# Optimization experiments

Measured on AMD Instinct MI355X. Metric: run time of the kernel, lower is better.

The kernel has to match this reference:

```python
import jax, jax.numpy as jnp
import numpy as np
from math import sqrt

H = 16  # num_heads
E = 1024  # embedding_size
B, S = 2, 2048

def setup_inputs() -> dict:
    key = jax.random.key(0)
    ks = jax.random.split(key, 12)
    sc = 1.0 / sqrt(E)
    inp = {
        'q': jax.random.normal(ks[0], (B, S, E), jnp.float32),
        'k': jax.random.normal(ks[1], (B, S, E), jnp.float32),
        'v': jax.random.normal(ks[2], (B, S, E), jnp.float32),
        'Wq': jax.random.normal(ks[3], (E, E), jnp.float32) * sc,
        'bq': jnp.zeros((E,), jnp.float32),
        'Wk': jax.random.normal(ks[4], (E, E), jnp.float32) * sc,
        'bk': jnp.zeros((E,), jnp.float32),
        'Wv': jax.random.normal(ks[5], (E, E), jnp.float32) * sc,
        'bv': jnp.zeros((E,), jnp.float32),
        'Wo': jax.random.normal(ks[6], (E, E), jnp.float32) * sc,
        'bo': jnp.zeros((E,), jnp.float32),
        'gamma': jnp.ones((E,), jnp.float32),
        'beta': jnp.zeros((E,), jnp.float32),
        'attn_mask': jnp.tril(jnp.ones((S, S), jnp.int32))[None, None],  # causal [1,1,S,S]
        'pad_mask': jnp.ones((B, S), jnp.int32),
    }
    return inp


def reference(q, k, v, Wq, bq, Wk, bk, Wv, bv, Wo, bo, gamma, beta, attn_mask, pad_mask):
    hs = E // H
    residual = q
    # NOTE: faithful to original: contiguous view(-1, H, S, hs) reinterprets
    # [B, S, E] memory directly as [B, H, S, hs] (no transpose).
    qh = (q @ Wq + bq).reshape(B, H, S, hs)
    kh = (k @ Wk + bk).reshape(B, H, S, hs)
    vh = (v @ Wv + bv).reshape(B, H, S, hs)
    scores = jnp.einsum('bhqd,bhkd->bhqk', qh, kh)  # [B,H,Sq,Sk]
    neg_inf = jnp.float32(-jnp.inf)
    scores = jnp.where(pad_mask[:, None, None, :] == 0, neg_inf, scores)
    scores = jnp.where(attn_mask == 0, neg_inf, scores)
    attn = jax.nn.softmax(scores / sqrt(hs), axis=-1)
    out = jnp.einsum('bhqk,bhkd->bhqd', attn, vh).reshape(B, S, E)
    out = out @ Wo + bo  # dropout is identity at inference
    x = residual + out
    mean = jnp.mean(x, axis=-1, keepdims=True)
    std = jnp.sqrt(jnp.mean((x - mean) ** 2, axis=-1, keepdims=True))  # unbiased=False
    return gamma * ((x - mean) / (std + 1e-8)) + beta
```

## Files before the change

### kernel.cpp

```cpp
#include <hip/hip_runtime.h>
#include <hip/hip_bf16.h>
#include <stdint.h>
#include <math.h>

#define NH 16
#define E_ 1024
#define B_ 2
#define S_ 2048
#define HS 64
#define M_TOT (B_*S_)

typedef __attribute__((ext_vector_type(4))) float f32x4;
typedef __attribute__((ext_vector_type(8))) short short8;

static __device__ __forceinline__ short f2bf(float f) {
    union { __hip_bfloat16 h; short s; } u;
    u.h = __float2bfloat16(f);
    return u.s;
}

static __device__ __forceinline__ void glds16(const void* g, void* l) {
    __builtin_amdgcn_global_load_lds(
        (__attribute__((address_space(1))) void*)(g),
        (__attribute__((address_space(3))) void*)(l),
        16, 0, 0);
}

__global__ __launch_bounds__(256) void cvt_qkv(
    const float* __restrict__ q, const float* __restrict__ k, const float* __restrict__ v,
    short* __restrict__ qb, short* __restrict__ kb, short* __restrict__ vb)
{
    const float* src; short* dst;
    if (blockIdx.y == 0)      { src = q; dst = qb; }
    else if (blockIdx.y == 1) { src = k; dst = kb; }
    else                      { src = v; dst = vb; }
    int i = (blockIdx.x * 256 + threadIdx.x) * 4;
    float4 f = *(const float4*)(src + i);
    short4 o;
    o.x = f2bf(f.x); o.y = f2bf(f.y); o.z = f2bf(f.z); o.w = f2bf(f.w);
    *(short4*)(dst + i) = o;
}

__global__ __launch_bounds__(256) void transpose_w4(
    const float* __restrict__ Wq, const float* __restrict__ Wk,
    const float* __restrict__ Wv, const float* __restrict__ Wo,
    short* __restrict__ Wqt, short* __restrict__ Wkt,
    short* __restrict__ Wvt, short* __restrict__ Wot)
{
    __shared__ float tile[32][33];
    const float* W; short* Wt;
    switch (blockIdx.z) {
        case 0: W = Wq; Wt = Wqt; break;
        case 1: W = Wk; Wt = Wkt; break;
        case 2: W = Wv; Wt = Wvt; break;
        default: W = Wo; Wt = Wot; break;
    }
    int tx = threadIdx.x, ty = threadIdx.y;
    int n0 = blockIdx.x * 32, k0 = blockIdx.y * 32;
#pragma unroll
    for (int i = 0; i < 4; i++)
        tile[ty + 8*i][tx] = W[(size_t)(k0 + ty + 8*i) * E_ + n0 + tx];
    __syncthreads();
#pragma unroll
    for (int i = 0; i < 4; i++)
        Wt[(size_t)(n0 + ty + 8*i) * E_ + k0 + tx] = f2bf(tile[tx][ty + 8*i]);
}

__global__ __launch_bounds__(256) void transpose_v(
    const short* __restrict__ Vb, short* __restrict__ Vt_g)
{
    __shared__ short tile[32][34];
    int tx = threadIdx.x, ty = threadIdx.y;
    int bh = blockIdx.z;
    int s0 = blockIdx.x * 32, d0 = blockIdx.y * 32;
    const short* src = Vb + (size_t)bh * S_ * HS;
    short* dst = Vt_g + (size_t)bh * HS * S_;
#pragma unroll
    for (int i = 0; i < 4; i++)
        tile[ty + 8*i][tx] = src[(size_t)(s0 + ty + 8*i) * HS + d0 + tx];
    __syncthreads();
#pragma unroll
    for (int i = 0; i < 4; i++)
        dst[(size_t)(d0 + ty + 8*i) * S_ + s0 + tx] = tile[tx][ty + 8*i];
}

#define BM 128
#define BN 128
#define BK 32

template<bool RESID>
__device__ __forceinline__ void gemm_core(
    const short* __restrict__ A, const short* __restrict__ Bt,
    const float* __restrict__ bias, const float* __restrict__ resid,
    short* __restrict__ outb, float* __restrict__ outf,
    int mblk, int nblk)
{
    __shared__ __align__(16) short As[BM * BK];
    __shared__ __align__(16) short Bs[BN * BK];

    const int tid  = threadIdx.x;
    const int lane = tid & 63;
    const int w    = tid >> 6;
    const int wm   = w >> 1, wn = w & 1;
    const int l15  = lane & 15, quad = lane >> 4;
    const int N = E_, K = E_;

    f32x4 acc[4][4];
#pragma unroll
    for (int i = 0; i < 4; i++)
#pragma unroll
        for (int j = 0; j < 4; j++)
            acc[i][j] = (f32x4){0.f, 0.f, 0.f, 0.f};

    const int arow = tid >> 2;
    const int acol = (tid & 3) * 8;
    const int m0 = mblk * BM, n0 = nblk * BN;
    short* AsW0 = As + w * 512;
    short* AsW1 = As + 2048 + w * 512;
    short* BsW0 = Bs + w * 512;
    short* BsW1 = Bs + 2048 + w * 512;

    for (int k0 = 0; k0 < K; k0 += BK) {
        __syncthreads();
        glds16(A  + (size_t)(m0 + arow)      * K + k0 + acol, AsW0);
        glds16(A  + (size_t)(m0 + arow + 64) * K + k0 + acol, AsW1);
        glds16(Bt + (size_t)(n0 + arow)      * K + k0 + acol, BsW0);
        glds16(Bt + (size_t)(n0 + arow + 64) * K + k0 + acol, BsW1);
        __syncthreads();

        short8 af[4], bf[4];
#pragma unroll
        for (int i = 0; i < 4; i++)
            af[i] = *(const short8*)(As + (wm*64 + i*16 + l15) * BK + quad*8);
#pragma unroll
        for (int j = 0; j < 4; j++)
            bf[j] = *(const short8*)(Bs + (wn*64 + j*16 + l15) * BK + quad*8);
#pragma unroll
        for (int i = 0; i < 4; i++)
#pragma unroll
            for (int j = 0; j < 4; j++)
                acc[i][j] = __builtin_amdgcn_mfma_f32_16x16x32_bf16(af[i], bf[j], acc[i][j], 0, 0, 0);
    }

#pragma unroll
    for (int i = 0; i < 4; i++)
#pragma unroll
        for (int j = 0; j < 4; j++) {
            int col = n0 + wn*64 + j*16 + l15;
            float bcol = bias[col];
#pragma unroll
            for (int r = 0; r < 4; r++) {
                int row = m0 + wm*64 + i*16 + quad*4 + r;
                float vv = acc[i][j][r] + bcol;
                if (RESID) {
                    outf[(size_t)row * N + col] = vv + resid[(size_t)row * N + col];
                } else {
                    outb[(size_t)row * N + col] = f2bf(vv);
                }
            }
        }
}

__global__ __launch_bounds__(256) void gemm_qkv(
    const short* qb, const short* kb, const short* vb,
    const short* Wqt, const short* Wkt, const short* Wvt,
    const float* bq, const float* bk, const float* bv,
    short* Qb, short* Kb, short* Vb)
{
    const short *A, *Bt; const float* bias; short* out;
    switch (blockIdx.z) {
        case 0:  A = qb; Bt = Wqt; bias = bq; out = Qb; break;
        case 1:  A = kb; Bt = Wkt; bias = bk; out = Kb; break;
        default: A = vb; Bt = Wvt; bias = bv; out = Vb; break;
    }
    gemm_core<false>(A, Bt, bias, nullptr, out, nullptr, blockIdx.y, blockIdx.x);
}

__global__ __launch_bounds__(256) void gemm_out(
    const short* Ab, const short* Wot, const float* bo,
    const float* resid, float* xout)
{
    gemm_core<true>(Ab, Wot, bo, resid, nullptr, xout, blockIdx.y, blockIdx.x);
}

#define SP 72

__global__ __launch_bounds__(256, 4) void flash_attn(
    const short* __restrict__ Q, const short* __restrict__ K,
    const short* __restrict__ Vt_g, short* __restrict__ O)
{
    const int bh  = blockIdx.y;
    const int qt  = (blockIdx.x + bh) & 31;
    const int tid = threadIdx.x;
    const int lane = tid & 63, w = tid >> 6;
    const int l15 = lane & 15, quad = lane >> 4;

    __shared__ __align__(16) short Ks[64 * SP];
    __shared__ __align__(16) short Vt[64 * SP];
    __shared__ __align__(16) short Ps[4][16 * SP];
    short* myPs = Ps[w];

    const short* Qbase = Q + ((size_t)bh * S_ + qt * 64 + w * 16) * HS;
    const short* Kb0   = K + (size_t)bh * S_ * HS;
    const short* Vg    = Vt_g + (size_t)bh * HS * S_;

    const int r0 = tid >> 3, c0 = (tid & 7) * 8;
    const int r1 = (tid + 256) >> 3, c1 = c0;

    short8 qf[2];
    qf[0] = *(const short8*)(Qbase + l15 * HS + quad * 8);
    qf[1] = *(const short8*)(Qbase + l15 * HS + 32 + quad * 8);

    uint4 rk0, rk1, rv0, rv1;
    {
        const short* Kt = Kb0;
        rk0 = *(const uint4*)(Kt + tid * 8);
        rk1 = *(const uint4*)(Kt + (tid + 256) * 8);
        rv0 = *(const uint4*)(Vg + (size_t)r0 * S_ + c0);
        rv1 = *(const uint4*)(Vg + (size_t)r1 * S_ + c1);
    }

    f32x4 o_acc[4];
#pragma unroll
    for (int j = 0; j < 4; j++) o_acc[j] = (f32x4){0.f, 0.f, 0.f, 0.f};
    float lsum[4] = {0.f, 0.f, 0.f, 0.f};

    for (int kt = 0; kt <= qt; kt++) {
        __syncthreads();
        *(uint4*)(Ks + r0 * SP + c0) = rk0;
        *(uint4*)(Ks + r1 * SP + c1) = rk1;
        *(uint4*)(Vt + r0 * SP + c0) = rv0;
        *(uint4*)(Vt + r1 * SP + c1) = rv1;
        __syncthreads();

        if (kt < qt) {
            const short* Kt = Kb0 + (size_t)(kt + 1) * 64 * HS;
            rk0 = *(const uint4*)(Kt + tid * 8);
            rk1 = *(const uint4*)(Kt + (tid + 256) * 8);
            rv0 = *(const uint4*)(Vg + (size_t)r0 * S_ + (kt + 1) * 64 + c0);
            rv1 = *(const uint4*)(Vg + (size_t)r1 * S_ + (kt + 1) * 64 + c1);
        }

        f32x4 sc[4];
#pragma unroll
        for (int j = 0; j < 4; j++) sc[j] = (f32x4){0.f, 0.f, 0.f, 0.f};
#pragma unroll
        for (int ks = 0; ks < 2; ks++)
#pragma unroll
            for (int j = 0; j < 4; j++) {
                short8 bk_ = *(const short8*)(Ks + (j*16 + l15) * SP + ks*32 + quad*8);
                sc[j] = __builtin_amdgcn_mfma_f32_16x16x32_bf16(qf[ks], bk_, sc[j], 0, 0, 0);
            }

        const bool diag = (kt == qt);
#pragma unroll
        for (int r = 0; r < 4; r++) {
            int qrow = w*16 + quad*4 + r;
            float rs = 0.f;
#pragma unroll
            for (int j = 0; j < 4; j++) {
                float s = sc[j][r] * 0.125f;
                if (diag) { int kc = j*16 + l15; if (kc > qrow) s = -INFINITY; }
                float p = __expf(s);
                rs += p;
                myPs[(quad*4 + r) * SP + j*16 + l15] = f2bf(p);
            }
            lsum[r] += rs;
        }

        short8 ap[2];
        ap[0] = *(const short8*)(myPs + l15 * SP + quad*8);
        ap[1] = *(const short8*)(myPs + l15 * SP + 32 + quad*8);
#pragma unroll
        for (int ks = 0; ks < 2; ks++)
#pragma unroll
            for (int j2 = 0; j2 < 4; j2++) {
                short8 bv_ = *(const short8*)(Vt + (j2*16 + l15) * SP + ks*32 + quad*8);
                o_acc[j2] = __builtin_amdgcn_mfma_f32_16x16x32_bf16(ap[ks], bv_, o_acc[j2], 0, 0, 0);
            }
    }

#pragma unroll
    for (int r = 0; r < 4; r++) {
#pragma unroll
        for (int off = 1; off < 16; off <<= 1)
            lsum[r] += __shfl_xor(lsum[r], off);
    }

    short* Ob = O + ((size_t)bh * S_ + qt * 64 + w * 16) * HS;
#pragma unroll
    for (int r = 0; r < 4; r++) {
        float inv = 1.f / lsum[r];
#pragma unroll
        for (int j2 = 0; j2 < 4; j2++)
            Ob[(quad*4 + r) * HS + j2*16 + l15] = f2bf(o_acc[j2][r] * inv);
    }
}

__global__ __launch_bounds__(256) void layernorm_k(
    const float* __restrict__ x, const float* __restrict__ gamma,
    const float* __restrict__ beta, float* __restrict__ out)
{
    int row = blockIdx.x;
    int tid = threadIdx.x;
    const float* xr = x + (size_t)row * E_;
    float4 v = *(const float4*)(xr + tid * 4);

    float s = v.x + v.y + v.z + v.w;
#pragma unroll
    for (int off = 1; off < 64; off <<= 1) s += __shfl_xor(s, off);
    __shared__ float red[4];
    if ((tid & 63) == 0) red[tid >> 6] = s;
    __syncthreads();
    float mean = (red[0] + red[1] + red[2] + red[3]) * (1.f / E_);

    float dx0 = v.x - mean, dx1 = v.y - mean, dx2 = v.z - mean, dx3 = v.w - mean;
    float sq = dx0*dx0 + dx1*dx1 + dx2*dx2 + dx3*dx3;
#pragma unroll
    for (int off = 1; off < 64; off <<= 1) sq += __shfl_xor(sq, off);
    __syncthreads();
    if ((tid & 63) == 0) red[tid >> 6] = sq;
    __syncthreads();
    float var = (red[0] + red[1] + red[2] + red[3]) * (1.f / E_);
    float inv = 1.f / (sqrtf(var) + 1e-8f);

    float4 g = *(const float4*)(gamma + tid * 4);
    float4 b = *(const float4*)(beta + tid * 4);
    float4 o;
    o.x = g.x * dx0 * inv + b.x;
    o.y = g.y * dx1 * inv + b.y;
    o.z = g.z * dx2 * inv + b.z;
    o.w = g.w * dx3 * inv + b.w;
    *(float4*)(out + (size_t)row * E_ + tid * 4) = o;
}

extern "C" void kernel_launch(void* const* d_in, const int* in_sizes, int n_in,
                              void* d_out, int out_size, void* d_ws, size_t ws_size,
                              hipStream_t stream)
{
    const float* q     = (const float*)d_in[0];
    const float* k     = (const float*)d_in[1];
    const float* v     = (const float*)d_in[2];
    const float* Wq    = (const float*)d_in[3];
    const float* bq    = (const float*)d_in[4];
    const float* Wk    = (const float*)d_in[5];
    const float* bk    = (const float*)d_in[6];
    const float* Wv    = (const float*)d_in[7];
    const float* bv    = (const float*)d_in[8];
    const float* Wo    = (const float*)d_in[9];
    const float* bo    = (const float*)d_in[10];
    const float* gamma = (const float*)d_in[11];
    const float* beta  = (const float*)d_in[12];

    const size_t ACT = (size_t)M_TOT * E_;
    char* ws = (char*)d_ws;
    size_t off = 0;
    auto alloc = [&](size_t bytes) { char* p = ws + off; off += bytes; return p; };

    short* qb   = (short*)alloc(ACT * 2);
    short* kb   = (short*)alloc(ACT * 2);
    short* vb   = (short*)alloc(ACT * 2);
    short* Wqt  = (short*)alloc((size_t)E_ * E_ * 2);
    short* Wkt  = (short*)alloc((size_t)E_ * E_ * 2);
    short* Wvt  = (short*)alloc((size_t)E_ * E_ * 2);
    short* Wot  = (short*)alloc((size_t)E_ * E_ * 2);
    short* Qb   = (short*)alloc(ACT * 2);
    short* Kb   = (short*)alloc(ACT * 2);
    short* Vb   = (short*)alloc(ACT * 2);
    short* Ob   = (short*)alloc(ACT * 2);
    float* xb   = (float*)alloc(ACT * 4);
    short* Vt_g = qb;

    cvt_qkv<<<dim3(ACT / 4 / 256, 3), 256, 0, stream>>>(q, k, v, qb, kb, vb);
    transpose_w4<<<dim3(32, 32, 4), dim3(32, 8), 0, stream>>>(Wq, Wk, Wv, Wo, Wqt, Wkt, Wvt, Wot);
    gemm_qkv<<<dim3(E_ / BN, M_TOT / BM, 3), 256, 0, stream>>>(qb, kb, vb, Wqt, Wkt, Wvt,
                                                               bq, bk, bv, Qb, Kb, Vb);
    transpose_v<<<dim3(S_ / 32, HS / 32, B_ * NH), dim3(32, 8), 0, stream>>>(Vb, Vt_g);
    flash_attn<<<dim3(S_ / 64, B_ * NH), 256, 0, stream>>>(Qb, Kb, Vt_g, Ob);
    gemm_out<<<dim3(E_ / BN, M_TOT / BM), 256, 0, stream>>>(Ob, Wot, bo, q, xb);
    layernorm_k<<<M_TOT, 256, 0, stream>>>(xb, gamma, beta, (float*)d_out);
}
```

Measured before the change: 265.3 us.

## Enlarge attention Q tile to 128 rows and split-K the output GEMM

Flash attention now handles 128 query rows per block, 32 per wave, so each K/V tile loaded into LDS feeds twice as many MFMAs. Query tiles are also reordered across heads to balance the causal workload, and fully masked tiles are skipped per wave. The output projection is split along K into two partial GEMMs that double the grid, with bias and residual addition moved into the layernorm kernel. The cost is more registers, with launch bounds lowered to two blocks per SM, plus an extra fp32 partial buffer read by layernorm.

```diff
diff --git a/kernel.cpp b/kernel.cpp
--- a/kernel.cpp
+++ b/kernel.cpp
@@ -88,12 +88,12 @@
 #define BN 128
 #define BK 32
 
-template<bool RESID>
+template<int MODE>
 __device__ __forceinline__ void gemm_core(
     const short* __restrict__ A, const short* __restrict__ Bt,
-    const float* __restrict__ bias, const float* __restrict__ resid,
+    const float* __restrict__ bias,
     short* __restrict__ outb, float* __restrict__ outf,
-    int mblk, int nblk)
+    int mblk, int nblk, int kbeg, int kend)
 {
     __shared__ __align__(16) short As[BM * BK];
     __shared__ __align__(16) short Bs[BN * BK];
@@ -120,7 +120,7 @@
     short* BsW0 = Bs + w * 512;
     short* BsW1 = Bs + 2048 + w * 512;
 
-    for (int k0 = 0; k0 < K; k0 += BK) {
+    for (int k0 = kbeg; k0 < kend; k0 += BK) {
         __syncthreads();
         glds16(A  + (size_t)(m0 + arow)      * K + k0 + acol, AsW0);
         glds16(A  + (size_t)(m0 + arow + 64) * K + k0 + acol, AsW1);
@@ -147,15 +147,14 @@
 #pragma unroll
         for (int j = 0; j < 4; j++) {
             int col = n0 + wn*64 + j*16 + l15;
-            float bcol = bias[col];
+            float bcol = (MODE == 0) ? bias[col] : 0.f;
 #pragma unroll
             for (int r = 0; r < 4; r++) {
                 int row = m0 + wm*64 + i*16 + quad*4 + r;
-                float vv = acc[i][j][r] + bcol;
-                if (RESID) {
-                    outf[(size_t)row * N + col] = vv + resid[(size_t)row * N + col];
+                if (MODE == 0) {
+                    outb[(size_t)row * N + col] = f2bf(acc[i][j][r] + bcol);
                 } else {
-                    outb[(size_t)row * N + col] = f2bf(vv);
+                    outf[(size_t)row * N + col] = acc[i][j][r];
                 }
             }
         }
@@ -173,138 +172,172 @@
         case 1:  A = kb; Bt = Wkt; bias = bk; out = Kb; break;
         default: A = vb; Bt = Wvt; bias = bv; out = Vb; break;
     }
-    gemm_core<false>(A, Bt, bias, nullptr, out, nullptr, blockIdx.y, blockIdx.x);
-}
-
-__global__ __launch_bounds__(256) void gemm_out(
-    const short* Ab, const short* Wot, const float* bo,
-    const float* resid, float* xout)
-{
-    gemm_core<true>(Ab, Wot, bo, resid, nullptr, xout, blockIdx.y, blockIdx.x);
+    gemm_core<0>(A, Bt, bias, out, nullptr, blockIdx.y, blockIdx.x, 0, E_);
+}
+
+__global__ __launch_bounds__(256) void gemm_out_sk(
+    const short* Ab, const short* Wot, float* xb0, float* xb1)
+{
+    float* out = (blockIdx.z == 0) ? xb0 : xb1;
+    int kbeg = blockIdx.z * (E_ / 2);
+    gemm_core<1>(Ab, Wot, nullptr, nullptr, out, blockIdx.y, blockIdx.x, kbeg, kbeg + E_/2);
 }
 
 #define SP 72
 
-__global__ __launch_bounds__(256, 4) void flash_attn(
+__global__ __launch_bounds__(256, 2) void flash_attn(
     const short* __restrict__ Q, const short* __restrict__ K,
     const short* __restrict__ Vt_g, short* __restrict__ O)
 {
-    const int bh  = blockIdx.y;
-    const int qt  = (blockIdx.x + bh) & 31;
-    const int tid = threadIdx.x;
+    const int bh   = blockIdx.y;
+    const int base = (blockIdx.x + bh) & 15;
+    const int qt   = (bh & 16) ? (15 - base) : base;
+    const int tid  = threadIdx.x;
     const int lane = tid & 63, w = tid >> 6;
-    const int l15 = lane & 15, quad = lane >> 4;
+    const int l15  = lane & 15, quad = lane >> 4;
 
     __shared__ __align__(16) short Ks[64 * SP];
     __shared__ __align__(16) short Vt[64 * SP];
-    __shared__ __align__(16) short Ps[4][16 * SP];
+    __shared__ __align__(16) short Ps[4][32 * SP];
     short* myPs = Ps[w];
 
-    const short* Qbase = Q + ((size_t)bh * S_ + qt * 64 + w * 16) * HS;
+    const int row0 = qt * 128 + w * 32;
+    const short* Qbase = Q + ((size_t)bh * S_ + row0) * HS;
     const short* Kb0   = K + (size_t)bh * S_ * HS;
     const short* Vg    = Vt_g + (size_t)bh * HS * S_;
 
     const int r0 = tid >> 3, c0 = (tid & 7) * 8;
-    const int r1 = (tid + 256) >> 3, c1 = c0;
-
-    short8 qf[2];
-    qf[0] = *(const short8*)(Qbase + l15 * HS + quad * 8);
-    qf[1] = *(const short8*)(Qbase + l15 * HS + 32 + quad * 8);
-
-    uint4 rk0, rk1, rv0, rv1;
-    {
-        const short* Kt = Kb0;
-        rk0 = *(const uint4*)(Kt + tid * 8);
-        rk1 = *(const uint4*)(Kt + (tid + 256) * 8);
-        rv0 = *(const uint4*)(Vg + (size_t)r0 * S_ + c0);
-        rv1 = *(const uint4*)(Vg + (size_t)r1 * S_ + c1);
-    }
-
-    f32x4 o_acc[4];
-#pragma unroll
-    for (int j = 0; j < 4; j++) o_acc[j] = (f32x4){0.f, 0.f, 0.f, 0.f};
-    float lsum[4] = {0.f, 0.f, 0.f, 0.f};
-
-    for (int kt = 0; kt <= qt; kt++) {
+    const int r1 = r0 + 32;
+
+    short8 qf[2][2];
+#pragma unroll
+    for (int i = 0; i < 2; i++) {
+        qf[i][0] = *(const short8*)(Qbase + (i*16 + l15) * HS + quad * 8);
+        qf[i][1] = *(const short8*)(Qbase + (i*16 + l15) * HS + 32 + quad * 8);
+    }
+
+    const int ktmax = 2 * qt + 1;
+
+    uint4 rk0 = *(const uint4*)(Kb0 + tid * 8);
+    uint4 rk1 = *(const uint4*)(Kb0 + (tid + 256) * 8);
+    uint4 rv0 = *(const uint4*)(Vg + (size_t)r0 * S_ + c0);
+    uint4 rv1 = *(const uint4*)(Vg + (size_t)r1 * S_ + c0);
+
+    f32x4 o_acc[2][4];
+#pragma unroll
+    for (int i = 0; i < 2; i++)
+#pragma unroll
+        for (int j = 0; j < 4; j++) o_acc[i][j] = (f32x4){0.f, 0.f, 0.f, 0.f};
+    float lsum[2][4] = {{0.f,0.f,0.f,0.f},{0.f,0.f,0.f,0.f}};
+
+    for (int kt = 0; kt <= ktmax; kt++) {
         __syncthreads();
         *(uint4*)(Ks + r0 * SP + c0) = rk0;
-        *(uint4*)(Ks + r1 * SP + c1) = rk1;
+        *(uint4*)(Ks + r1 * SP + c0) = rk1;
         *(uint4*)(Vt + r0 * SP + c0) = rv0;
-        *(uint4*)(Vt + r1 * SP + c1) = rv1;
+        *(uint4*)(Vt + r1 * SP + c0) = rv1;
         __syncthreads();
 
-        if (kt < qt) {
+        if (kt < ktmax) {
             const short* Kt = Kb0 + (size_t)(kt + 1) * 64 * HS;
             rk0 = *(const uint4*)(Kt + tid * 8);
             rk1 = *(const uint4*)(Kt + (tid + 256) * 8);
             rv0 = *(const uint4*)(Vg + (size_t)r0 * S_ + (kt + 1) * 64 + c0);
-            rv1 = *(const uint4*)(Vg + (size_t)r1 * S_ + (kt + 1) * 64 + c1);
+            rv1 = *(const uint4*)(Vg + (size_t)r1 * S_ + (kt + 1) * 64 + c0);
         }
 
-        f32x4 sc[4];
-#pragma unroll
-        for (int j = 0; j < 4; j++) sc[j] = (f32x4){0.f, 0.f, 0.f, 0.f};
+        if (kt * 64 > row0 + 31) continue;
+
+        f32x4 sc[2][4];
+#pragma unroll
+        for (int i = 0; i < 2; i++)
+#pragma unroll
+            for (int j = 0; j < 4; j++) sc[i][j] = (f32x4){0.f, 0.f, 0.f, 0.f};
 #pragma unroll
         for (int ks = 0; ks < 2; ks++)
 #pragma unroll
             for (int j = 0; j < 4; j++) {
-                short8 bk_ = *(const short8*)(Ks + (j*16 + l15) * SP + ks*32 + quad*8);
-                sc[j] = __builtin_amdgcn_mfma_f32_16x16x32_bf16(qf[ks], bk_, sc[j], 0, 0, 0);
+                short8 kf = *(const short8*)(Ks + (j*16 + l15) * SP + ks*32 + quad*8);
+#pragma unroll
+                for (int i = 0; i < 2; i++)
+                    sc[i][j] = __builtin_amdgcn_mfma_f32_16x16x32_bf16(qf[i][ks], kf, sc[i][j], 0, 0, 0);
             }
 
-        const bool diag = (kt == qt);
+        const bool needmask = (kt * 64 + 63) > row0;
+#pragma unroll
+        for (int i = 0; i < 2; i++)
+#pragma unroll
+            for (int r = 0; r < 4; r++) {
+                int qrow = row0 + i*16 + quad*4 + r;
+                float rs = 0.f;
+#pragma unroll
+                for (int j = 0; j < 4; j++) {
+                    float s = sc[i][j][r] * 0.125f;
+                    if (needmask) { int kc = kt*64 + j*16 + l15; if (kc > qrow) s = -INFINITY; }
+                    float p = __expf(s);
+                    rs += p;
+                    myPs[(i*16 + quad*4 + r) * SP + j*16 + l15] = f2bf(p);
+                }
+                lsum[i][r] += rs;
+            }
+
+        short8 ap[2][2];
+#pragma unroll
+        for (int i = 0; i < 2; i++) {
+            ap[i][0] = *(const short8*)(myPs + (i*16 + l15) * SP + quad*8);
+            ap[i][1] = *(const short8*)(myPs + (i*16 + l15) * SP + 32 + quad*8);
+        }
+#pragma unroll
+        for (int ks = 0; ks < 2; ks++)
+#pragma unroll
+            for (int j2 = 0; j2 < 4; j2++) {
+                short8 vf = *(const short8*)(Vt + (j2*16 + l15) * SP + ks*32 + quad*8);
+#pragma unroll
+                for (int i = 0; i < 2; i++)
+                    o_acc[i][j2] = __builtin_amdgcn_mfma_f32_16x16x32_bf16(ap[i][ks], vf, o_acc[i][j2], 0, 0, 0);
+            }
+    }
+
+#pragma unroll
+    for (int i = 0; i < 2; i++)
 #pragma unroll
         for (int r = 0; r < 4; r++) {
-            int qrow = w*16 + quad*4 + r;
-            float rs = 0.f;
-#pragma unroll
-            for (int j = 0; j < 4; j++) {
-                float s = sc[j][r] * 0.125f;
-                if (diag) { int kc = j*16 + l15; if (kc > qrow) s = -INFINITY; }
-                float p = __expf(s);
-                rs += p;
-                myPs[(quad*4 + r) * SP + j*16 + l15] = f2bf(p);
-            }
-            lsum[r] += rs;
+#pragma unroll
+            for (int off = 1; off < 16; off <<= 1)
+                lsum[i][r] += __shfl_xor(lsum[i][r], off);
         }
 
-        short8 ap[2];
-        ap[0] = *(const short8*)(myPs + l15 * SP + quad*8);
-        ap[1] = *(const short8*)(myPs + l15 * SP + 32 + quad*8);
-#pragma unroll
-        for (int ks = 0; ks < 2; ks++)
-#pragma unroll
-            for (int j2 = 0; j2 < 4; j2++) {
-                short8 bv_ = *(const short8*)(Vt + (j2*16 + l15) * SP + ks*32 + quad*8);
-                o_acc[j2] = __builtin_amdgcn_mfma_f32_16x16x32_bf16(ap[ks], bv_, o_acc[j2], 0, 0, 0);
-            }
-    }
-
-#pragma unroll
-    for (int r = 0; r < 4; r++) {
-#pragma unroll
-        for (int off = 1; off < 16; off <<= 1)
-            lsum[r] += __shfl_xor(lsum[r], off);
-    }
-
-    short* Ob = O + ((size_t)bh * S_ + qt * 64 + w * 16) * HS;
-#pragma unroll
-    for (int r = 0; r < 4; r++) {
-        float inv = 1.f / lsum[r];
-#pragma unroll
-        for (int j2 = 0; j2 < 4; j2++)
-            Ob[(quad*4 + r) * HS + j2*16 + l15] = f2bf(o_acc[j2][r] * inv);
+#pragma unroll
+    for (int i = 0; i < 2; i++) {
+        short* Ob = O + ((size_t)bh * S_ + row0 + i*16) * HS;
+#pragma unroll
+        for (int r = 0; r < 4; r++) {
+            float inv = 1.f / lsum[i][r];
+#pragma unroll
+            for (int j2 = 0; j2 < 4; j2++)
+                Ob[(quad*4 + r) * HS + j2*16 + l15] = f2bf(o_acc[i][j2][r] * inv);
+        }
     }
 }
 
 __global__ __launch_bounds__(256) void layernorm_k(
-    const float* __restrict__ x, const float* __restrict__ gamma,
-    const float* __restrict__ beta, float* __restrict__ out)
+    const float* __restrict__ xb0, const float* __restrict__ xb1,
+    const float* __restrict__ resid, const float* __restrict__ bo,
+    const float* __restrict__ gamma, const float* __restrict__ beta,
+    float* __restrict__ out)
 {
     int row = blockIdx.x;
     int tid = threadIdx.x;
-    const float* xr = x + (size_t)row * E_;
-    float4 v = *(const float4*)(xr + tid * 4);
+    size_t o4 = (size_t)row * E_ + tid * 4;
+    float4 a = *(const float4*)(xb0 + o4);
+    float4 b2 = *(const float4*)(xb1 + o4);
+    float4 c = *(const float4*)(resid + o4);
+    float4 d = *(const float4*)(bo + tid * 4);
+    float4 v;
+    v.x = a.x + b2.x + c.x + d.x;
+    v.y = a.y + b2.y + c.y + d.y;
+    v.z = a.z + b2.z + c.z + d.z;
+    v.w = a.w + b2.w + c.w + d.w;
 
     float s = v.x + v.y + v.z + v.w;
 #pragma unroll
@@ -331,7 +364,7 @@
     o.y = g.y * dx1 * inv + b.y;
     o.z = g.z * dx2 * inv + b.z;
     o.w = g.w * dx3 * inv + b.w;
-    *(float4*)(out + (size_t)row * E_ + tid * 4) = o;
+    *(float4*)(out + o4) = o;
 }
 
 extern "C" void kernel_launch(void* const* d_in, const int* in_sizes, int n_in,
@@ -368,15 +401,16 @@
     short* Kb   = (short*)alloc(ACT * 2);
     short* Vb   = (short*)alloc(ACT * 2);
     short* Ob   = (short*)alloc(ACT * 2);
-    float* xb   = (float*)alloc(ACT * 4);
-    short* Vt_g = qb;
+    float* xb0  = (float*)alloc(ACT * 4);
+    short* Vt_g = vb;
+    float* xb1  = (float*)qb;
 
     cvt_qkv<<<dim3(ACT / 4 / 256, 3), 256, 0, stream>>>(q, k, v, qb, kb, vb);
     transpose_w4<<<dim3(32, 32, 4), dim3(32, 8), 0, stream>>>(Wq, Wk, Wv, Wo, Wqt, Wkt, Wvt, Wot);
     gemm_qkv<<<dim3(E_ / BN, M_TOT / BM, 3), 256, 0, stream>>>(qb, kb, vb, Wqt, Wkt, Wvt,
                                                                bq, bk, bv, Qb, Kb, Vb);
     transpose_v<<<dim3(S_ / 32, HS / 32, B_ * NH), dim3(32, 8), 0, stream>>>(Vb, Vt_g);
-    flash_attn<<<dim3(S_ / 64, B_ * NH), 256, 0, stream>>>(Qb, Kb, Vt_g, Ob);
-    gemm_out<<<dim3(E_ / BN, M_TOT / BM), 256, 0, stream>>>(Ob, Wot, bo, q, xb);
-    layernorm_k<<<M_TOT, 256, 0, stream>>>(xb, gamma, beta, (float*)d_out);
-}
+    flash_attn<<<dim3(S_ / 128, B_ * NH), 256, 0, stream>>>(Qb, Kb, Vt_g, Ob);
+    gemm_out_sk<<<dim3(E_ / BN, M_TOT / BM, 2), 256, 0, stream>>>(Ob, Wot, xb0, xb1);
+    layernorm_k<<<M_TOT, 256, 0, stream>>>(xb0, xb1, q, bo, gamma, beta, (float*)d_out);
+}
```

Measured after the change: 267.9 us. Within noise of the previous version (+1.0%).

## Fuse fp32-to-bf16 conversion into QKV GEMM, split-K output GEMM, balance causal tiles

Applied to the files above, without the earlier changes.

Removes the separate cvt_qkv kernel by having the QKV GEMM load fp32 activations and convert them to bf16 in registers before writing them to LDS. The output projection is split along K into two halves, doubling block count, and the partial sums, bias and residual are combined inside the layernorm kernel. The flash-attention query-tile order is permuted to pair short and long causal tiles for better load balance. The trade-off is that the A-operand path now uses synchronous register loads instead of direct global-to-LDS loads, and the layernorm reads extra fp32 partial buffers.

```diff
diff --git a/kernel.cpp b/kernel.cpp
--- a/kernel.cpp
+++ b/kernel.cpp
@@ -24,21 +24,6 @@
         (__attribute__((address_space(1))) void*)(g),
         (__attribute__((address_space(3))) void*)(l),
         16, 0, 0);
-}
-
-__global__ __launch_bounds__(256) void cvt_qkv(
-    const float* __restrict__ q, const float* __restrict__ k, const float* __restrict__ v,
-    short* __restrict__ qb, short* __restrict__ kb, short* __restrict__ vb)
-{
-    const float* src; short* dst;
-    if (blockIdx.y == 0)      { src = q; dst = qb; }
-    else if (blockIdx.y == 1) { src = k; dst = kb; }
-    else                      { src = v; dst = vb; }
-    int i = (blockIdx.x * 256 + threadIdx.x) * 4;
-    float4 f = *(const float4*)(src + i);
-    short4 o;
-    o.x = f2bf(f.x); o.y = f2bf(f.y); o.z = f2bf(f.z); o.w = f2bf(f.w);
-    *(short4*)(dst + i) = o;
 }
 
 __global__ __launch_bounds__(256) void transpose_w4(
@@ -88,12 +73,12 @@
 #define BN 128
 #define BK 32
 
-template<bool RESID>
+template<int MODE, bool AF32>
 __device__ __forceinline__ void gemm_core(
-    const short* __restrict__ A, const short* __restrict__ Bt,
-    const float* __restrict__ bias, const float* __restrict__ resid,
+    const void* __restrict__ Ap, const short* __restrict__ Bt,
+    const float* __restrict__ bias,
     short* __restrict__ outb, float* __restrict__ outf,
-    int mblk, int nblk)
+    int mblk, int nblk, int kbeg, int kend)
 {
     __shared__ __align__(16) short As[BM * BK];
     __shared__ __align__(16) short Bs[BN * BK];
@@ -120,10 +105,30 @@
     short* BsW0 = Bs + w * 512;
     short* BsW1 = Bs + 2048 + w * 512;
 
-    for (int k0 = 0; k0 < K; k0 += BK) {
+    const float* Af = (const float*)Ap;
+    const short* Ab = (const short*)Ap;
+
+    for (int k0 = kbeg; k0 < kend; k0 += BK) {
+        float4 fa0, fa1, fb0, fb1;
+        if (AF32) {
+            fa0 = *(const float4*)(Af + (size_t)(m0 + arow)      * K + k0 + acol);
+            fa1 = *(const float4*)(Af + (size_t)(m0 + arow)      * K + k0 + acol + 4);
+            fb0 = *(const float4*)(Af + (size_t)(m0 + arow + 64) * K + k0 + acol);
+            fb1 = *(const float4*)(Af + (size_t)(m0 + arow + 64) * K + k0 + acol + 4);
+        }
         __syncthreads();
-        glds16(A  + (size_t)(m0 + arow)      * K + k0 + acol, AsW0);
-        glds16(A  + (size_t)(m0 + arow + 64) * K + k0 + acol, AsW1);
+        if (AF32) {
+            short8 s0, s1;
+            s0[0]=f2bf(fa0.x); s0[1]=f2bf(fa0.y); s0[2]=f2bf(fa0.z); s0[3]=f2bf(fa0.w);
+            s0[4]=f2bf(fa1.x); s0[5]=f2bf(fa1.y); s0[6]=f2bf(fa1.z); s0[7]=f2bf(fa1.w);
+            s1[0]=f2bf(fb0.x); s1[1]=f2bf(fb0.y); s1[2]=f2bf(fb0.z); s1[3]=f2bf(fb0.w);
+            s1[4]=f2bf(fb1.x); s1[5]=f2bf(fb1.y); s1[6]=f2bf(fb1.z); s1[7]=f2bf(fb1.w);
+            *(short8*)(As + arow * BK + acol)        = s0;
+            *(short8*)(As + (arow + 64) * BK + acol) = s1;
+        } else {
+            glds16(Ab + (size_t)(m0 + arow)      * K + k0 + acol, AsW0);
+            glds16(Ab + (size_t)(m0 + arow + 64) * K + k0 + acol, AsW1);
+        }
         glds16(Bt + (size_t)(n0 + arow)      * K + k0 + acol, BsW0);
         glds16(Bt + (size_t)(n0 + arow + 64) * K + k0 + acol, BsW1);
         __syncthreads();
@@ -147,40 +152,40 @@
 #pragma unroll
         for (int j = 0; j < 4; j++) {
             int col = n0 + wn*64 + j*16 + l15;
-            float bcol = bias[col];
+            float bcol = (MODE == 0) ? bias[col] : 0.f;
 #pragma unroll
             for (int r = 0; r < 4; r++) {
                 int row = m0 + wm*64 + i*16 + quad*4 + r;
-                float vv = acc[i][j][r] + bcol;
-                if (RESID) {
-                    outf[(size_t)row * N + col] = vv + resid[(size_t)row * N + col];
+                if (MODE == 0) {
+                    outb[(size_t)row * N + col] = f2bf(acc[i][j][r] + bcol);
                 } else {
-                    outb[(size_t)row * N + col] = f2bf(vv);
+                    outf[(size_t)row * N + col] = acc[i][j][r];
                 }
             }
         }
 }
 
 __global__ __launch_bounds__(256) void gemm_qkv(
-    const short* qb, const short* kb, const short* vb,
+    const float* q, const float* k, const float* v,
     const short* Wqt, const short* Wkt, const short* Wvt,
     const float* bq, const float* bk, const float* bv,
     short* Qb, short* Kb, short* Vb)
 {
-    const short *A, *Bt; const float* bias; short* out;
+    const float* A; const short* Bt; const float* bias; short* out;
     switch (blockIdx.z) {
-        case 0:  A = qb; Bt = Wqt; bias = bq; out = Qb; break;
-        case 1:  A = kb; Bt = Wkt; bias = bk; out = Kb; break;
-        default: A = vb; Bt = Wvt; bias = bv; out = Vb; break;
-    }
-    gemm_core<false>(A, Bt, bias, nullptr, out, nullptr, blockIdx.y, blockIdx.x);
-}
-
-__global__ __launch_bounds__(256) void gemm_out(
-    const short* Ab, const short* Wot, const float* bo,
-    const float* resid, float* xout)
-{
-    gemm_core<true>(Ab, Wot, bo, resid, nullptr, xout, blockIdx.y, blockIdx.x);
+        case 0:  A = q; Bt = Wqt; bias = bq; out = Qb; break;
+        case 1:  A = k; Bt = Wkt; bias = bk; out = Kb; break;
+        default: A = v; Bt = Wvt; bias = bv; out = Vb; break;
+    }
+    gemm_core<0, true>(A, Bt, bias, out, nullptr, blockIdx.y, blockIdx.x, 0, E_);
+}
+
+__global__ __launch_bounds__(256) void gemm_out_sk(
+    const short* Ab, const short* Wot, float* xb0, float* xb1)
+{
+    float* out = (blockIdx.z == 0) ? xb0 : xb1;
+    int kbeg = blockIdx.z * (E_ / 2);
+    gemm_core<1, false>(Ab, Wot, nullptr, nullptr, out, blockIdx.y, blockIdx.x, kbeg, kbeg + E_/2);
 }
 
 #define SP 72
@@ -190,7 +195,9 @@
     const short* __restrict__ Vt_g, short* __restrict__ O)
 {
     const int bh  = blockIdx.y;
-    const int qt  = (blockIdx.x + bh) & 31;
+    const int u   = (blockIdx.x + bh) & 31;
+    const int ua  = u & 7, ub = u >> 3;
+    const int qt  = (ub == 0) ? ua : (ub == 1) ? 15 - ua : (ub == 2) ? 16 + ua : 31 - ua;
     const int tid = threadIdx.x;
     const int lane = tid & 63, w = tid >> 6;
     const int l15 = lane & 15, quad = lane >> 4;
@@ -298,13 +305,23 @@
 }
 
 __global__ __launch_bounds__(256) void layernorm_k(
-    const float* __restrict__ x, const float* __restrict__ gamma,
-    const float* __restrict__ beta, float* __restrict__ out)
+    const float* __restrict__ xb0, const float* __restrict__ xb1,
+    const float* __restrict__ resid, const float* __restrict__ bo,
+    const float* __restrict__ gamma, const float* __restrict__ beta,
+    float* __restrict__ out)
 {
     int row = blockIdx.x;
     int tid = threadIdx.x;
-    const float* xr = x + (size_t)row * E_;
-    float4 v = *(const float4*)(xr + tid * 4);
+    size_t o4 = (size_t)row * E_ + tid * 4;
+    float4 a = *(const float4*)(xb0 + o4);
+    float4 b2 = *(const float4*)(xb1 + o4);
+    float4 c = *(const float4*)(resid + o4);
+    float4 d = *(const float4*)(bo + tid * 4);
+    float4 v;
+    v.x = a.x + b2.x + c.x + d.x;
+    v.y = a.y + b2.y + c.y + d.y;
+    v.z = a.z + b2.z + c.z + d.z;
+    v.w = a.w + b2.w + c.w + d.w;
 
     float s = v.x + v.y + v.z + v.w;
 #pragma unroll
@@ -331,7 +348,7 @@
     o.y = g.y * dx1 * inv + b.y;
     o.z = g.z * dx2 * inv + b.z;
     o.w = g.w * dx3 * inv + b.w;
-    *(float4*)(out + (size_t)row * E_ + tid * 4) = o;
+    *(float4*)(out + o4) = o;
 }
 
 extern "C" void kernel_launch(void* const* d_in, const int* in_sizes, int n_in,
@@ -357,9 +374,6 @@
     size_t off = 0;
     auto alloc = [&](size_t bytes) { char* p = ws + off; off += bytes; return p; };
 
-    short* qb   = (short*)alloc(ACT * 2);
-    short* kb   = (short*)alloc(ACT * 2);
-    short* vb   = (short*)alloc(ACT * 2);
     short* Wqt  = (short*)alloc((size_t)E_ * E_ * 2);
     short* Wkt  = (short*)alloc((size_t)E_ * E_ * 2);
     short* Wvt  = (short*)alloc((size_t)E_ * E_ * 2);
@@ -367,16 +381,16 @@
     short* Qb   = (short*)alloc(ACT * 2);
     short* Kb   = (short*)alloc(ACT * 2);
     short* Vb   = (short*)alloc(ACT * 2);
+    short* Vt_g = (short*)alloc(ACT * 2);
     short* Ob   = (short*)alloc(ACT * 2);
-    float* xb   = (float*)alloc(ACT * 4);
-    short* Vt_g = qb;
-
-    cvt_qkv<<<dim3(ACT / 4 / 256, 3), 256, 0, stream>>>(q, k, v, qb, kb, vb);
+    float* xb0  = (float*)alloc(ACT * 4);
+    float* xb1  = (float*)Qb;
+
     transpose_w4<<<dim3(32, 32, 4), dim3(32, 8), 0, stream>>>(Wq, Wk, Wv, Wo, Wqt, Wkt, Wvt, Wot);
-    gemm_qkv<<<dim3(E_ / BN, M_TOT / BM, 3), 256, 0, stream>>>(qb, kb, vb, Wqt, Wkt, Wvt,
+    gemm_qkv<<<dim3(E_ / BN, M_TOT / BM, 3), 256, 0, stream>>>(q, k, v, Wqt, Wkt, Wvt,
                                                                bq, bk, bv, Qb, Kb, Vb);
     transpose_v<<<dim3(S_ / 32, HS / 32, B_ * NH), dim3(32, 8), 0, stream>>>(Vb, Vt_g);
     flash_attn<<<dim3(S_ / 64, B_ * NH), 256, 0, stream>>>(Qb, Kb, Vt_g, Ob);
-    gemm_out<<<dim3(E_ / BN, M_TOT / BM), 256, 0, stream>>>(Ob, Wot, bo, q, xb);
-    layernorm_k<<<M_TOT, 256, 0, stream>>>(xb, gamma, beta, (float*)d_out);
-}
+    gemm_out_sk<<<dim3(E_ / BN, M_TOT / BM, 2), 256, 0, stream>>>(Ob, Wot, xb0, xb1);
+    layernorm_k<<<M_TOT, 256, 0, stream>>>(xb0, xb1, q, bo, gamma, beta, (float*)d_out);
+}
```

New measurement: 264.0 us. No clear change (-0.5%).
